# Kernel optimization log

Hardware: AMD Instinct MI355X
Metric: run time of the kernel (lower is better)

## Reference

```python
import jax, jax.numpy as jnp
import numpy as np

B, T, C = 16, 4096, 128
K, STRIDE, BLANK = 5, 1, 0
NEG = -1e30
LEXICON = [[c] for c in range(1, 27)] + [[c, c + 1] for c in range(1, 27)]


def _build_tables():
    # Replicates make_kernel_graph(x, blank_idx=0, blank_optional=True, spike=False)
    arcs_list, accept_list, n_states = [], [], []
    for tok in LEXICON:
        arcs = [(0, 0, BLANK)]  # blank self-loop at start
        n = len(tok)
        for i, c in enumerate(tok):
            arcs.append((2 * i, 2 * i + 1, c))
            arcs.append((2 * i + 1, 2 * i + 1, c))      # spike=False: label self-loop
            arcs.append((2 * i + 1, 2 * i + 2, BLANK))
            arcs.append((2 * i + 2, 2 * i + 2, BLANK))
            if i > 0 and tok[i - 1] != c:               # blank_optional skip arc
                arcs.append((2 * i - 1, 2 * i + 1, c))
        S = 2 * n + 1
        acc = np.zeros(S, bool)
        acc[2 * n] = True
        if n > 0:
            acc[2 * n - 1] = True                        # blank_optional accept
        arcs_list.append(arcs); accept_list.append(acc); n_states.append(S)
    Kn = len(LEXICON)
    A = max(len(a) for a in arcs_list)
    S = max(n_states)
    SRC = np.zeros((Kn, A), np.int32); DST = np.zeros((Kn, A), np.int32)
    LAB = np.zeros((Kn, A), np.int32); VAL = np.zeros((Kn, A), bool)
    ACC = np.zeros((Kn, S), bool)
    for k, arcs in enumerate(arcs_list):
        for a, (s, d, l) in enumerate(arcs):
            SRC[k, a], DST[k, a], LAB[k, a], VAL[k, a] = s, d, l, True
        ACC[k, :n_states[k]] = accept_list[k]
    return jnp.array(SRC), jnp.array(DST), jnp.array(LAB), jnp.array(VAL), jnp.array(ACC), S

SRC, DST, LAB, VAL, ACC, S_MAX = _build_tables()


def _step(alpha, em, src, dst, lab, val):
    # One time-step of the forward algorithm over the kernel automaton.
    # alpha [B,W,S], em [B,W,C]; src/dst/lab/val [A]
    contrib = jnp.where(val, alpha[..., src] + em[..., lab], NEG)          # [B,W,A]
    m = jnp.full(alpha.shape, NEG, alpha.dtype).at[..., dst].max(contrib)  # segment max
    e = jnp.where(val, jnp.exp(contrib - m[..., dst]), 0.0)
    s = jnp.zeros_like(alpha).at[..., dst].add(e)                          # segment sum
    return jnp.where(s > 0, m + jnp.log(jnp.maximum(s, 1e-30)), NEG)


def _forward(x):
    pad = K // 2
    xp = jnp.pad(x, ((0, 0), (pad, pad), (0, 0)))  # F.pad on time dim
    W = (T + 2 * pad - K) // STRIDE + 1            # number of sliding windows
    starts = jnp.arange(W) * STRIDE
    Kn = SRC.shape[0]
    alpha0 = jnp.full((Kn, x.shape[0], W, S_MAX), NEG, x.dtype).at[..., 0].set(0.0)

    def body(alpha, t):
        em = xp[:, starts + t, :]                   # [B,W,C] emissions at window step t
        alpha = jax.vmap(_step, in_axes=(0, None, 0, 0, 0, 0))(alpha, em, SRC, DST, LAB, VAL)
        return alpha, None

    alpha, _ = jax.lax.scan(body, alpha0, jnp.arange(K))
    # forward_score = logsumexp over accepting states
    vals = jnp.where(ACC[:, None, None, :], alpha, NEG)                    # [Kn,B,W,S]
    m = vals.max(-1)
    out = m + jnp.log(jnp.sum(jnp.exp(vals - m[..., None]), -1))
    # scale='none' (divide by 1.0), normalize='none'
    return jnp.transpose(out, (1, 2, 0))                                   # [B,W,Kn]


def setup_inputs() -> dict:
    key = jax.random.key(0)
    x = jax.random.normal(key, (B, T, C), jnp.float32)
    return {"x": x}


def reference(x):
    return _forward(x)
```

## Files before the change

### kernel.cpp

```cpp
#include <hip/hip_runtime.h>


constexpr int TFRM  = 4096;
constexpr int CCH   = 128;
constexpr int WN    = 4096;
constexpr int KN    = 52;
constexpr int BB    = 16;

constexpr int WTILE  = 64;
constexpr int NTH    = 256;
constexpr int FRAMES = WTILE + 4;
constexpr int CH     = 28;
constexpr int LDSTR  = 29;

__global__ __launch_bounds__(NTH)
void conv_transduce_kernel(const float* __restrict__ x, float* __restrict__ out) {
    __shared__ float E[FRAMES * LDSTR];

    const int b  = blockIdx.y;
    const int w0 = blockIdx.x * WTILE;

    for (int i = threadIdx.x; i < FRAMES * CH; i += NTH) {
        const int f  = i / CH;
        const int ch = i - f * CH;
        const int g  = w0 + f - 2;
        float v = 0.0f;
        if (g >= 0 && g < TFRM)
            v = x[(size_t)(b * TFRM + g) * CCH + ch];
        E[f * LDSTR + ch] = __expf(v);
    }
    __syncthreads();

    const int wl = threadIdx.x & 63;
    const int p  = threadIdx.x >> 6;
    const int w  = w0 + wl;

    float E0[5];
    #pragma unroll
    for (int t = 0; t < 5; ++t) E0[t] = E[(wl + t) * LDSTR + 0];

    float* __restrict__ orow = out + (size_t)(b * WN + w) * KN;

    for (int j = p; j < 27; j += 4) {
        const int c = j + 1;
        float Ec[5];
        #pragma unroll
        for (int t = 0; t < 5; ++t) Ec[t] = E[(wl + t) * LDSTR + c];

        if (c <= 26) {
            float p0 = 1.0f, p1 = 0.0f, p2 = 0.0f;
            #pragma unroll
            for (int t = 0; t < 5; ++t) {
                const float n0 = p0 * E0[t];
                const float n1 = (p0 + p1) * Ec[t];
                const float n2 = (p1 + p2) * E0[t];
                p0 = n0; p1 = n1; p2 = n2;
            }
            orow[c - 1] = __logf(p1 + p2);
        }
        if (c >= 2) {
            float Ea[5];
            #pragma unroll
            for (int t = 0; t < 5; ++t) Ea[t] = E[(wl + t) * LDSTR + (c - 1)];
            float q0 = 1.0f, q1 = 0.0f, q2 = 0.0f, q3 = 0.0f, q4 = 0.0f;
            #pragma unroll
            for (int t = 0; t < 5; ++t) {
                const float s01 = q0 + q1;
                const float s12 = q1 + q2;
                const float n0 = q0 * E0[t];
                const float n1 = s01 * Ea[t];
                const float n2 = s12 * E0[t];
                const float n3 = (s12 + q3) * Ec[t];
                const float n4 = (q3 + q4) * E0[t];
                q0 = n0; q1 = n1; q2 = n2; q3 = n3; q4 = n4;
            }
            orow[24 + c] = __logf(q3 + q4);
        }
    }
}

extern "C" void kernel_launch(void* const* d_in, const int* in_sizes, int n_in,
                              void* d_out, int out_size, void* d_ws, size_t ws_size,
                              hipStream_t stream) {
    (void)in_sizes; (void)n_in; (void)d_ws; (void)ws_size; (void)out_size;
    const float* x = (const float*)d_in[0];
    float* out = (float*)d_out;
    dim3 grid(WN / WTILE, BB);
    conv_transduce_kernel<<<grid, NTH, 0, stream>>>(x, out);
}
```

Baseline: 89.68 us.

## Vectorize input loads, share single-token recurrence, stage outputs in LDS for coalesced stores

Input frames are now loaded as float4 vectors (7 per frame covering channels 0-27), replacing scalar loads. The single-character token score is read from the prefix states of the two-character automaton, so the separate 3-state recurrence is dropped. Outputs are written to a shared-memory tile and then stored contiguously by the whole block, replacing strided per-thread row writes. This uses extra LDS and a second barrier, which may lower occupancy.

```diff
diff --git a/kernel.cpp b/kernel.cpp
--- a/kernel.cpp
+++ b/kernel.cpp
@@ -10,72 +10,71 @@
 constexpr int WTILE  = 64;
 constexpr int NTH    = 256;
 constexpr int FRAMES = WTILE + 4;
-constexpr int CH     = 28;
 constexpr int LDSTR  = 29;
+constexpr int OSTR   = 53;
 
 __global__ __launch_bounds__(NTH)
 void conv_transduce_kernel(const float* __restrict__ x, float* __restrict__ out) {
     __shared__ float E[FRAMES * LDSTR];
+    __shared__ float O[WTILE * OSTR];
 
     const int b  = blockIdx.y;
     const int w0 = blockIdx.x * WTILE;
 
-    for (int i = threadIdx.x; i < FRAMES * CH; i += NTH) {
-        const int f  = i / CH;
-        const int ch = i - f * CH;
-        const int g  = w0 + f - 2;
-        float v = 0.0f;
-        if (g >= 0 && g < TFRM)
-            v = x[(size_t)(b * TFRM + g) * CCH + ch];
-        E[f * LDSTR + ch] = __expf(v);
+    for (int i = threadIdx.x; i < FRAMES * 7; i += NTH) {
+        const int f = i / 7;
+        const int v = i - f * 7;
+        const int g = w0 + f - 2;
+        float* dst = &E[f * LDSTR + v * 4];
+        if (g >= 0 && g < TFRM) {
+            const float4 val = *reinterpret_cast<const float4*>(
+                x + (size_t)(b * TFRM + g) * CCH + v * 4);
+            dst[0] = __expf(val.x);
+            dst[1] = __expf(val.y);
+            dst[2] = __expf(val.z);
+            dst[3] = __expf(val.w);
+        } else {
+            dst[0] = 1.0f; dst[1] = 1.0f; dst[2] = 1.0f; dst[3] = 1.0f;
+        }
     }
     __syncthreads();
 
     const int wl = threadIdx.x & 63;
     const int p  = threadIdx.x >> 6;
-    const int w  = w0 + wl;
 
     float E0[5];
     #pragma unroll
     for (int t = 0; t < 5; ++t) E0[t] = E[(wl + t) * LDSTR + 0];
 
-    float* __restrict__ orow = out + (size_t)(b * WN + w) * KN;
+    for (int a = p + 1; a <= 26; a += 4) {
+        float Ea[5], Eb[5];
+        #pragma unroll
+        for (int t = 0; t < 5; ++t) Ea[t] = E[(wl + t) * LDSTR + a];
+        #pragma unroll
+        for (int t = 0; t < 5; ++t) Eb[t] = E[(wl + t) * LDSTR + a + 1];
 
-    for (int j = p; j < 27; j += 4) {
-        const int c = j + 1;
-        float Ec[5];
+        float q0 = 1.0f, q1 = 0.0f, q2 = 0.0f, q3 = 0.0f, q4 = 0.0f;
         #pragma unroll
-        for (int t = 0; t < 5; ++t) Ec[t] = E[(wl + t) * LDSTR + c];
+        for (int t = 0; t < 5; ++t) {
+            const float s01 = q0 + q1;
+            const float s12 = q1 + q2;
+            const float n0 = q0 * E0[t];
+            const float n1 = s01 * Ea[t];
+            const float n2 = s12 * E0[t];
+            const float n3 = (s12 + q3) * Eb[t];
+            const float n4 = (q3 + q4) * E0[t];
+            q0 = n0; q1 = n1; q2 = n2; q3 = n3; q4 = n4;
+        }
+        O[wl * OSTR + (a - 1)]  = __logf(q1 + q2);
+        O[wl * OSTR + (25 + a)] = __logf(q3 + q4);
+    }
+    __syncthreads();
 
-        if (c <= 26) {
-            float p0 = 1.0f, p1 = 0.0f, p2 = 0.0f;
-            #pragma unroll
-            for (int t = 0; t < 5; ++t) {
-                const float n0 = p0 * E0[t];
-                const float n1 = (p0 + p1) * Ec[t];
-                const float n2 = (p1 + p2) * E0[t];
-                p0 = n0; p1 = n1; p2 = n2;
-            }
-            orow[c - 1] = __logf(p1 + p2);
-        }
-        if (c >= 2) {
-            float Ea[5];
-            #pragma unroll
-            for (int t = 0; t < 5; ++t) Ea[t] = E[(wl + t) * LDSTR + (c - 1)];
-            float q0 = 1.0f, q1 = 0.0f, q2 = 0.0f, q3 = 0.0f, q4 = 0.0f;
-            #pragma unroll
-            for (int t = 0; t < 5; ++t) {
-                const float s01 = q0 + q1;
-                const float s12 = q1 + q2;
-                const float n0 = q0 * E0[t];
-                const float n1 = s01 * Ea[t];
-                const float n2 = s12 * E0[t];
-                const float n3 = (s12 + q3) * Ec[t];
-                const float n4 = (q3 + q4) * E0[t];
-                q0 = n0; q1 = n1; q2 = n2; q3 = n3; q4 = n4;
-            }
-            orow[24 + c] = __logf(q3 + q4);
-        }
+    float* __restrict__ oblk = out + ((size_t)b * WN + w0) * KN;
+    for (int i = threadIdx.x; i < WTILE * KN; i += NTH) {
+        const int wi = i / KN;
+        const int k  = i - wi * KN;
+        oblk[i] = O[wi * OSTR + k];
     }
 }
 
```

New measurement: 77.66 us. -13.4%, faster.
